# Optimization experiments

Measured on AMD Instinct MI355X. Metric: run time of the kernel, lower is better.

## Reference

```python
import jax, jax.numpy as jnp
import numpy as np

R = 15  # receptive-field rows (self.rfield)
_NAMES = ['1x', '2x', '3x', '4x', '1e', '2e', '3e', '4e', '5', '6', '7', '8', '9']
_CIN = [3, 64, 64, 64, 3, 64, 64, 64, 64, 64, 64, 64, 64]
_COUT = [64, 64, 64, 64, 64, 64, 64, 64, 64, 64, 64, 64, 3]


def _leaky(x):
    return jnp.where(x >= 0, x, 0.01 * x)  # nn.LeakyReLU default slope


def _conv(x, w, b, ph):
    # 3x3 conv, stride 1, padding (ph, 1) matching torch Conv2d padding=[ph, 1]
    y = jax.lax.conv_general_dilated(x, w, (1, 1), ((ph, ph), (1, 1)),
                                     dimension_numbers=('NCHW', 'OIHW', 'NCHW'))
    return y + b[None, :, None, None]


def setup_inputs():
    key = jax.random.key(0)
    ks = jax.random.split(key, len(_NAMES) + 1)
    inp = {'x': jax.random.normal(ks[0], (1, 3, 31, 256), jnp.float32)}
    for j, n in enumerate(_NAMES):
        std = np.float32((2.0 / (_CIN[j] * 9)) ** 0.5)  # He init for 3x3 conv
        inp['w' + n] = jax.random.normal(ks[j + 1], (_COUT[j], _CIN[j], 3, 3), jnp.float32) * std
        inp['b' + n] = jnp.zeros((_COUT[j],), jnp.float32)
    return inp


def _predict(s, e, p):
    # x-branch: 15 rows -> 9 rows (three H-valid convs)
    for n, ph in (('1x', 1), ('2x', 0), ('3x', 0), ('4x', 0)):
        s = _leaky(_conv(s, p['w' + n], p['b' + n], ph))
    # e-branch
    for n, ph in (('1e', 1), ('2e', 0), ('3e', 0), ('4e', 0)):
        e = _leaky(_conv(e, p['w' + n], p['b' + n], ph))
    B, C, Hs, W = s.shape  # C == 64 -> per-pixel 8x8 matrices; Hs == R - 6 == 9
    sr = jnp.transpose(s, (0, 2, 3, 1)).reshape(B, Hs, W, 8, 8)
    er = jnp.transpose(e, (0, 2, 3, 1)).reshape(B, Hs, W, 8, 8)
    pr = jnp.einsum('bhwij,bhwjk->bhwik', er, sr).reshape(B, Hs, W, 64)
    pr = jnp.transpose(pr, (0, 3, 1, 2))  # [B,64,9,W]
    # fuse stack: 9 rows -> 1 row, then 64 -> 3 channels
    for n, ph in (('5', 0), ('6', 0), ('7', 0), ('8', 0), ('9', 1)):
        pr = _leaky(_conv(pr, p['w' + n], p['b' + n], ph))
    return pr  # [B, 3, 1, W]


def _forward(x, p):
    B, C, H, W = x.shape

    def step(ebuf, i):
        # torch code sets error = x (alias), so slice_x and slice_e are the SAME mutated buffer
        sl = jax.lax.dynamic_slice(ebuf, (0, 0, i, 0), (B, C, R, W))
        pr = _predict(sl, sl, p)
        # act_row reads row ky of the (mutated) x, but row ky is overwritten only after this read,
        # so it still equals the original input row
        act = jax.lax.dynamic_slice(x, (0, 0, i + R, 0), (B, C, 1, W))
        ebuf = jax.lax.dynamic_update_slice(ebuf, act - pr, (0, 0, i + R, 0))
        return ebuf, pr

    ebuf, preds = jax.lax.scan(step, x, jnp.arange(H - R))
    pred = jnp.transpose(preds[:, :, :, 0, :], (1, 2, 0, 3))  # [S,B,C,1,W] -> [B,C,S,W]
    # 'truth' is read from the in-place-mutated x, i.e. the residual buffer, matching the torch aliasing bug/behavior
    truth = ebuf[:, :, R:, :]
    return pred, truth


def reference(x, w1x, b1x, w2x, b2x, w3x, b3x, w4x, b4x, w1e, b1e, w2e, b2e, w3e, b3e, w4e, b4e, w5, b5, w6, b6, w7, b7, w8, b8, w9, b9):
    p = dict(w1x=w1x, b1x=b1x, w2x=w2x, b2x=b2x, w3x=w3x, b3x=b3x, w4x=w4x, b4x=b4x,
             w1e=w1e, b1e=b1e, w2e=w2e, b2e=b2e, w3e=w3e, b3e=b3e, w4e=w4e, b4e=b4e,
             w5=w5, b5=b5, w6=w6, b6=b6, w7=w7, b7=b7, w8=w8, b8=b8, w9=w9, b9=b9)
    return _forward(x, p)
```

## Files before the change

### kernel.cpp

```cpp
#include <hip/hip_runtime.h>

#define LEAKY(v) ((v) >= 0.f ? (v) : 0.01f * (v))

#define CS   4608
#define ZS1  294912
#define TSL  16
#define BSL  17
#define EBCS 7936

struct JobD { const float* t0; const float* t1; const float* t2; float* o; };
struct IncP { JobD jd[6]; };

__global__ __launch_bounds__(256, 2) void convInc(
    IncP P, const float* __restrict__ W0, const float* __restrict__ B0,
    const float* __restrict__ W1, const float* __restrict__ B1,
    int zsel, int ics, int ocs)
{
    const int lane = threadIdx.x;
    const int y    = threadIdx.y;
    const int q    = blockIdx.x >> 6;
    const int cout = blockIdx.x & 63;
    const int z    = (zsel >> q) & 1;
    const float* W  = (z ? W1 : W0) + cout * 576 + y * 144;
    const float* Bv = z ? B1 : B0;
    const JobD jd  = P.jd[q];
    const int yo   = y * 16 * ics + lane * 4;
    const float* t0 = jd.t0 + yo;
    const float* t1 = jd.t1 + yo;
    const float* t2 = jd.t2 + yo;

    float acc[4] = {};
    #pragma unroll 4
    for (int c = 0; c < 16; ++c) {
        #pragma unroll
        for (int t = 0; t < 3; ++t) {
            const float* rp = (t == 0 ? t0 : (t == 1 ? t1 : t2)) + c * ics;
            float4 v = *(const float4*)rp;
            float wl = __shfl_up(v.w, 1);   if (lane == 0)  wl = 0.f;
            float wr = __shfl_down(v.x, 1); if (lane == 63) wr = 0.f;
            const float win[6] = {wl, v.x, v.y, v.z, v.w, wr};
            const float* wj = W + c * 9 + t * 3;
            #pragma unroll
            for (int cc = 0; cc < 4; ++cc)
                acc[cc] += wj[0] * win[cc] + wj[1] * win[cc + 1] + wj[2] * win[cc + 2];
        }
    }

    __shared__ float red[4][256];
    *(float4*)&red[y][lane * 4] = *(float4*)acc;
    __syncthreads();
    const int col = y * 64 + lane;
    float v = Bv[cout] + red[0][col] + red[1][col] + red[2][col] + red[3][col];
    jd.o[cout * ocs + col] = LEAKY(v);
}

struct C3P { const float* t[3][3]; float* o[3][2]; };

__global__ __launch_bounds__(256, 2) void conv3inc(
    C3P P, const float* __restrict__ W0, const float* __restrict__ B0,
    const float* __restrict__ W1, const float* __restrict__ B1)
{
    const int lane = threadIdx.x & 63;
    const int wv   = threadIdx.x >> 6;
    const int job  = blockIdx.x >> 3;
    const int cq   = blockIdx.x & 3;
    const int z    = (blockIdx.x >> 2) & 1;
    const int cout0 = __builtin_amdgcn_readfirstlane(cq * 16 + wv * 4);
    const float* W  = (z ? W1 : W0) + cout0 * 27;
    const float* Bv = z ? B1 : B0;

    float a[4][4] = {};
    #pragma unroll
    for (int t = 0; t < 3; ++t) {
        const float* rp = P.t[job][t];
        if (rp) {
            #pragma unroll
            for (int c = 0; c < 3; ++c) {
                float4 v = *(const float4*)(rp + c * EBCS + lane * 4);
                float wl = __shfl_up(v.w, 1);   if (lane == 0)  wl = 0.f;
                float wr = __shfl_down(v.x, 1); if (lane == 63) wr = 0.f;
                const float win[6] = {wl, v.x, v.y, v.z, v.w, wr};
                #pragma unroll
                for (int j = 0; j < 4; ++j) {
                    const float* wj = W + j * 27 + c * 9 + t * 3;
                    #pragma unroll
                    for (int cc = 0; cc < 4; ++cc)
                        a[j][cc] += wj[0] * win[cc] + wj[1] * win[cc + 1] + wj[2] * win[cc + 2];
                }
            }
        }
    }
    float* o = P.o[job][z];
    #pragma unroll
    for (int j = 0; j < 4; ++j) {
        const float bb = Bv[cout0 + j];
        float4 r4;
        r4.x = LEAKY(a[j][0] + bb); r4.y = LEAKY(a[j][1] + bb);
        r4.z = LEAKY(a[j][2] + bb); r4.w = LEAKY(a[j][3] + bb);
        *(float4*)(o + (cout0 + j) * CS + lane * 4) = r4;
    }
}

__global__ __launch_bounds__(256, 2) void conv3B(
    const float* __restrict__ ebuf,
    const float* __restrict__ W0, const float* __restrict__ B0,
    const float* __restrict__ W1, const float* __restrict__ B1,
    float* __restrict__ out)
{
    const int lane = threadIdx.x & 63;
    const int wv   = threadIdx.x >> 6;
    const int h  = blockIdx.y;
    const int cq = blockIdx.z & 3;
    const int z  = blockIdx.z >> 2;
    const int cout0 = __builtin_amdgcn_readfirstlane(cq * 16 + wv * 4);
    const float* W  = (z ? W1 : W0) + cout0 * 27;
    const float* Bv = z ? B1 : B0;

    float a[4][4] = {};
    #pragma unroll
    for (int kh = 0; kh < 3; ++kh) {
        const int r = h - 1 + kh;
        const bool valid = (r >= 0 && r < 15);
        const float msk = valid ? 1.f : 0.f;
        #pragma unroll
        for (int c = 0; c < 3; ++c) {
            const float* rr = ebuf + c * EBCS + (valid ? r : 0) * 256 + lane * 4;
            float4 v = *(const float4*)rr;
            v.x *= msk; v.y *= msk; v.z *= msk; v.w *= msk;
            float wl = __shfl_up(v.w, 1);   if (lane == 0)  wl = 0.f;
            float wr = __shfl_down(v.x, 1); if (lane == 63) wr = 0.f;
            const float win[6] = {wl, v.x, v.y, v.z, v.w, wr};
            #pragma unroll
            for (int j = 0; j < 4; ++j) {
                const float* wj = W + j * 27 + c * 9 + kh * 3;
                #pragma unroll
                for (int cc = 0; cc < 4; ++cc)
                    a[j][cc] += wj[0] * win[cc] + wj[1] * win[cc + 1] + wj[2] * win[cc + 2];
            }
        }
    }
    const int slot = (h == 0) ? TSL : (h == 14 ? BSL : (h & 15));
    float* o = out + (size_t)z * ZS1 + slot * 256;
    #pragma unroll
    for (int j = 0; j < 4; ++j) {
        const float bb = Bv[cout0 + j];
        float4 r4;
        r4.x = LEAKY(a[j][0] + bb); r4.y = LEAKY(a[j][1] + bb);
        r4.z = LEAKY(a[j][2] + bb); r4.w = LEAKY(a[j][3] + bb);
        *(float4*)(o + (cout0 + j) * CS + lane * 4) = r4;
    }
}

template<int HOUT, int HIN, int OFFI, int OFFO, int NZ>
__global__ __launch_bounds__(256, 2) void convYB(
    const float* __restrict__ in,
    const float* __restrict__ W0, const float* __restrict__ B0,
    const float* __restrict__ W1, const float* __restrict__ B1,
    float* __restrict__ out)
{
    const int lane = threadIdx.x;
    const int y    = threadIdx.y;
    const int h  = blockIdx.y;
    const int gz = blockIdx.z;
    const int z    = (NZ == 2) ? (gz >> 6) : 0;
    const int cout = (NZ == 2) ? (gz & 63) : gz;
    const float* W  = (z ? W1 : W0) + cout * 576 + y * 144;
    const float* Bv = z ? B1 : B0;
    const float* ib = in + (size_t)z * ZS1 + y * 16 * CS + lane * 4;

    int slot[3];
    #pragma unroll
    for (int t = 0; t < 3; ++t) {
        const int g = h + t;
        slot[t] = (g == 0) ? TSL : (g == HIN - 1 ? BSL : ((g + OFFI) & 15));
    }

    float acc[4] = {};
    #pragma unroll 4
    for (int c = 0; c < 16; ++c) {
        #pragma unroll
        for (int t = 0; t < 3; ++t) {
            float4 v = *(const float4*)(ib + c * CS + slot[t] * 256);
            float wl = __shfl_up(v.w, 1);   if (lane == 0)  wl = 0.f;
            float wr = __shfl_down(v.x, 1); if (lane == 63) wr = 0.f;
            const float win[6] = {wl, v.x, v.y, v.z, v.w, wr};
            const float* wj = W + c * 9 + t * 3;
            #pragma unroll
            for (int cc = 0; cc < 4; ++cc)
                acc[cc] += wj[0] * win[cc] + wj[1] * win[cc + 1] + wj[2] * win[cc + 2];
        }
    }

    __shared__ float red[4][256];
    *(float4*)&red[y][lane * 4] = *(float4*)acc;
    __syncthreads();
    const int col = y * 64 + lane;
    const int os = (h == 0) ? TSL : (h == HOUT - 1 ? BSL : ((h + OFFO) & 15));
    float v = Bv[cout] + red[0][col] + red[1][col] + red[2][col] + red[3][col];
    out[(size_t)z * ZS1 + cout * CS + os * 256 + col] = LEAKY(v);
}

__global__ __launch_bounds__(256, 2) void mmB(const float* __restrict__ L4R,
                                              float* __restrict__ MMR)
{
    const int col = threadIdx.x;
    const int r   = blockIdx.x;
    const int ig  = blockIdx.y;
    const int slot = (r == 0) ? TSL : (r == 8 ? BSL : ((r + 3) & 15));
    const float* s = L4R + slot * 256 + col;
    const float* e = L4R + ZS1 + slot * 256 + col;
    float sv[64];
    #pragma unroll
    for (int c = 0; c < 64; ++c) sv[c] = s[c * CS];
    float ev[8];
    #pragma unroll
    for (int j = 0; j < 8; ++j) ev[j] = e[(ig * 8 + j) * CS];
    #pragma unroll
    for (int k = 0; k < 8; ++k) {
        float acc = 0.f;
        #pragma unroll
        for (int j = 0; j < 8; ++j) acc += ev[j] * sv[j * 8 + k];
        MMR[(ig * 8 + k) * CS + slot * 256 + col] = acc;
    }
}

struct MMP { const float* s[3]; const float* e[3]; float* o[3]; };
__global__ __launch_bounds__(256, 2) void mminc(MMP P)
{
    const int col = threadIdx.x;
    const int job = blockIdx.x;
    const int ig  = blockIdx.y;
    const float* s = P.s[job] + col;
    const float* e = P.e[job] + col;
    float sv[64];
    #pragma unroll
    for (int c = 0; c < 64; ++c) sv[c] = s[c * CS];
    float ev[8];
    #pragma unroll
    for (int j = 0; j < 8; ++j) ev[j] = e[(ig * 8 + j) * CS];
    float* o = P.o[job];
    #pragma unroll
    for (int k = 0; k < 8; ++k) {
        float acc = 0.f;
        #pragma unroll
        for (int j = 0; j < 8; ++j) acc += ev[j] * sv[j * 8 + k];
        o[(ig * 8 + k) * CS + col] = acc;
    }
}

__global__ void conv9up(const float* __restrict__ pin, const float* __restrict__ w9,
                        const float* __restrict__ b9, const float* __restrict__ x,
                        float* __restrict__ ebuf, float* __restrict__ preds, int i)
{
    const int wcol = threadIdx.x;
    const int yq   = threadIdx.y;
    const int c0   = yq * 16;
    const bool mL = (wcol > 0), mR = (wcol < 255);
    float a0 = 0.f, a1 = 0.f, a2 = 0.f;

    #pragma unroll 4
    for (int c = 0; c < 16; ++c) {
        const int cin = c0 + c;
        const float* r_ = pin + cin * 256;
        float vm = mL ? r_[wcol - 1] : 0.f;
        float v0 = r_[wcol];
        float vp = mR ? r_[wcol + 1] : 0.f;
        const float* wk0 = w9 + (0 * 64 + cin) * 9 + 3;
        const float* wk1 = w9 + (1 * 64 + cin) * 9 + 3;
        const float* wk2 = w9 + (2 * 64 + cin) * 9 + 3;
        a0 += vm * wk0[0] + v0 * wk0[1] + vp * wk0[2];
        a1 += vm * wk1[0] + v0 * wk1[1] + vp * wk1[2];
        a2 += vm * wk2[0] + v0 * wk2[1] + vp * wk2[2];
    }

    __shared__ float red[4][3][256];
    red[yq][0][wcol] = a0;
    red[yq][1][wcol] = a1;
    red[yq][2][wcol] = a2;
    __syncthreads();

    if (yq == 0) {
        #pragma unroll
        for (int j = 0; j < 3; ++j) {
            float v = b9[j] + red[0][j][wcol] + red[1][j][wcol]
                            + red[2][j][wcol] + red[3][j][wcol];
            v = LEAKY(v);
            preds[i * 768 + j * 256 + wcol] = v;
            ebuf[j * EBCS + (15 + i) * 256 + wcol] =
                x[j * EBCS + (15 + i) * 256 + wcol] - v;
        }
    }
}

__global__ void finalize(const float* __restrict__ preds, const float* __restrict__ ebuf,
                         float* __restrict__ o)
{
    const int idx = blockIdx.x * 256 + threadIdx.x;
    if (idx >= 24576) return;
    if (idx < 12288) {
        const int c = idx >> 12;
        const int t = (idx >> 8) & 15;
        const int w = idx & 255;
        o[idx] = preds[t * 768 + c * 256 + w];
    } else {
        const int j = idx - 12288;
        const int c = j >> 12;
        const int t = (j >> 8) & 15;
        const int w = j & 255;
        o[idx] = ebuf[c * EBCS + (15 + t) * 256 + w];
    }
}

extern "C" void kernel_launch(void* const* d_in, const int* in_sizes, int n_in,
                              void* d_out, int out_size, void* d_ws, size_t ws_size,
                              hipStream_t stream)
{
    const float* x   = (const float*)d_in[0];
    const float* w1x = (const float*)d_in[1];  const float* b1x = (const float*)d_in[2];
    const float* w2x = (const float*)d_in[3];  const float* b2x = (const float*)d_in[4];
    const float* w3x = (const float*)d_in[5];  const float* b3x = (const float*)d_in[6];
    const float* w4x = (const float*)d_in[7];  const float* b4x = (const float*)d_in[8];
    const float* w1e = (const float*)d_in[9];  const float* b1e = (const float*)d_in[10];
    const float* w2e = (const float*)d_in[11]; const float* b2e = (const float*)d_in[12];
    const float* w3e = (const float*)d_in[13]; const float* b3e = (const float*)d_in[14];
    const float* w4e = (const float*)d_in[15]; const float* b4e = (const float*)d_in[16];
    const float* w5  = (const float*)d_in[17]; const float* b5  = (const float*)d_in[18];
    const float* w6  = (const float*)d_in[19]; const float* b6  = (const float*)d_in[20];
    const float* w7  = (const float*)d_in[21]; const float* b7  = (const float*)d_in[22];
    const float* w8  = (const float*)d_in[23]; const float* b8  = (const float*)d_in[24];
    const float* w9  = (const float*)d_in[25]; const float* b9  = (const float*)d_in[26];

    float* ws    = (float*)d_ws;
    float* ebuf  = ws;
    float* L1R   = ebuf + 23808;
    float* L2R   = L1R + 589824;
    float* L3R   = L2R + 589824;
    float* L4R   = L3R + 589824;
    float* MMR   = L4R + 589824;
    float* L5R   = MMR + 294912;
    float* L6R   = L5R + 294912;
    float* L7b   = L6R + 294912;
    float* L8b   = L7b + 49152;
    float* preds = L8b + 16384;

    auto S2 = [](int c) { return c & 15; };
    auto r2 = [](float* b, int z, int slot) { return b + (size_t)z * ZS1 + slot * 256; };
    auto r1 = [](float* b, int slot) { return b + slot * 256; };

    hipMemcpyAsync(ebuf, x, 23808 * sizeof(float), hipMemcpyDeviceToDevice, stream);

    const dim3 cb(64, 4);

    conv3B<<<dim3(1, 15, 8), 256, 0, stream>>>(ebuf, w1x, b1x, w1e, b1e, L1R);
    convYB<13, 15, 0, 1, 2><<<dim3(1, 13, 128), cb, 0, stream>>>(L1R, w2x, b2x, w2e, b2e, L2R);
    convYB<11, 13, 1, 2, 2><<<dim3(1, 11, 128), cb, 0, stream>>>(L2R, w3x, b3x, w3e, b3e, L3R);
    convYB<9, 11, 2, 3, 2><<<dim3(1, 9, 128), cb, 0, stream>>>(L3R, w4x, b4x, w4e, b4e, L4R);
    mmB<<<dim3(9, 8), 256, 0, stream>>>(L4R, MMR);
    convYB<7, 9, 3, 4, 1><<<dim3(1, 7, 64), cb, 0, stream>>>(MMR, w5, b5, w5, b5, L5R);
    convYB<5, 7, 4, 5, 1><<<dim3(1, 5, 64), cb, 0, stream>>>(L5R, w6, b6, w6, b6, L6R);

    for (int i = 0; i < 16; ++i) {
        if (i > 0) {
            C3P p3 = {};
            p3.t[0][0] = nullptr;                p3.t[0][1] = ebuf + i * 256;        p3.t[0][2] = ebuf + (i + 1) * 256;
            p3.t[1][0] = ebuf + (i + 13) * 256;  p3.t[1][1] = ebuf + (i + 14) * 256; p3.t[1][2] = nullptr;
            p3.t[2][0] = ebuf + (i + 12) * 256;  p3.t[2][1] = ebuf + (i + 13) * 256; p3.t[2][2] = ebuf + (i + 14) * 256;
            for (int z = 0; z < 2; ++z) {
                p3.o[0][z] = r2(L1R, z, TSL);
                p3.o[1][z] = r2(L1R, z, BSL);
                p3.o[2][z] = r2(L1R, z, S2(i + 13));
            }
            conv3inc<<<24, 256, 0, stream>>>(p3, w1x, b1x, w1e, b1e);

            IncP p2 = {};
            for (int z = 0; z < 2; ++z) {
                p2.jd[0 * 2 + z] = { r2(L1R, z, TSL),        r2(L1R, z, S2(i + 1)),  r2(L1R, z, S2(i + 2)),  r2(L2R, z, TSL) };
                p2.jd[1 * 2 + z] = { r2(L1R, z, S2(i + 12)), r2(L1R, z, S2(i + 13)), r2(L1R, z, BSL),        r2(L2R, z, BSL) };
                p2.jd[2 * 2 + z] = { r2(L1R, z, S2(i + 11)), r2(L1R, z, S2(i + 12)), r2(L1R, z, S2(i + 13)), r2(L2R, z, S2(i + 12)) };
            }
            convInc<<<384, cb, 0, stream>>>(p2, w2x, b2x, w2e, b2e, 42, CS, CS);

            IncP p3i = {};
            for (int z = 0; z < 2; ++z) {
                p3i.jd[0 * 2 + z] = { r2(L2R, z, TSL),        r2(L2R, z, S2(i + 2)),  r2(L2R, z, S2(i + 3)),  r2(L3R, z, TSL) };
                p3i.jd[1 * 2 + z] = { r2(L2R, z, S2(i + 11)), r2(L2R, z, S2(i + 12)), r2(L2R, z, BSL),        r2(L3R, z, BSL) };
                p3i.jd[2 * 2 + z] = { r2(L2R, z, S2(i + 10)), r2(L2R, z, S2(i + 11)), r2(L2R, z, S2(i + 12)), r2(L3R, z, S2(i + 11)) };
            }
            convInc<<<384, cb, 0, stream>>>(p3i, w3x, b3x, w3e, b3e, 42, CS, CS);

            IncP p4 = {};
            for (int z = 0; z < 2; ++z) {
                p4.jd[0 * 2 + z] = { r2(L3R, z, TSL),        r2(L3R, z, S2(i + 3)),  r2(L3R, z, S2(i + 4)),  r2(L4R, z, TSL) };
                p4.jd[1 * 2 + z] = { r2(L3R, z, S2(i + 10)), r2(L3R, z, S2(i + 11)), r2(L3R, z, BSL),        r2(L4R, z, BSL) };
                p4.jd[2 * 2 + z] = { r2(L3R, z, S2(i + 9)),  r2(L3R, z, S2(i + 10)), r2(L3R, z, S2(i + 11)), r2(L4R, z, S2(i + 10)) };
            }
            convInc<<<384, cb, 0, stream>>>(p4, w4x, b4x, w4e, b4e, 42, CS, CS);

            MMP pm;
            pm.s[0] = r2(L4R, 0, TSL);        pm.e[0] = r2(L4R, 1, TSL);        pm.o[0] = r1(MMR, TSL);
            pm.s[1] = r2(L4R, 0, BSL);        pm.e[1] = r2(L4R, 1, BSL);        pm.o[1] = r1(MMR, BSL);
            pm.s[2] = r2(L4R, 0, S2(i + 10)); pm.e[2] = r2(L4R, 1, S2(i + 10)); pm.o[2] = r1(MMR, S2(i + 10));
            mminc<<<dim3(3, 8), 256, 0, stream>>>(pm);

            IncP p5 = {};
            p5.jd[0] = { r1(MMR, TSL),       r1(MMR, S2(i + 4)),  r1(MMR, S2(i + 5)),  r1(L5R, TSL) };
            p5.jd[1] = { r1(MMR, S2(i + 9)), r1(MMR, S2(i + 10)), r1(MMR, BSL),        r1(L5R, BSL) };
            p5.jd[2] = { r1(MMR, S2(i + 8)), r1(MMR, S2(i + 9)),  r1(MMR, S2(i + 10)), r1(L5R, S2(i + 9)) };
            convInc<<<192, cb, 0, stream>>>(p5, w5, b5, w5, b5, 0, CS, CS);

            IncP p6 = {};
            p6.jd[0] = { r1(L5R, TSL),       r1(L5R, S2(i + 5)), r1(L5R, S2(i + 6)), r1(L6R, TSL) };
            p6.jd[1] = { r1(L5R, S2(i + 8)), r1(L5R, S2(i + 9)), r1(L5R, BSL),       r1(L6R, BSL) };
            p6.jd[2] = { r1(L5R, S2(i + 7)), r1(L5R, S2(i + 8)), r1(L5R, S2(i + 9)), r1(L6R, S2(i + 8)) };
            convInc<<<192, cb, 0, stream>>>(p6, w6, b6, w6, b6, 0, CS, CS);
        }

        IncP p7 = {};
        p7.jd[0] = { r1(L6R, TSL),       r1(L6R, S2(i + 6)), r1(L6R, S2(i + 7)), L7b };
        p7.jd[1] = { r1(L6R, S2(i + 6)), r1(L6R, S2(i + 7)), r1(L6R, S2(i + 8)), L7b + 256 };
        p7.jd[2] = { r1(L6R, S2(i + 7)), r1(L6R, S2(i + 8)), r1(L6R, BSL),       L7b + 512 };
        convInc<<<192, cb, 0, stream>>>(p7, w7, b7, w7, b7, 0, CS, 768);

        IncP p8 = {};
        p8.jd[0] = { L7b, L7b + 256, L7b + 512, L8b };
        convInc<<<64, cb, 0, stream>>>(p8, w8, b8, w8, b8, 0, 768, 256);

        conv9up<<<dim3(1, 1, 1), dim3(256, 4), 0, stream>>>(L8b, w9, b9, x, ebuf, preds, i);
    }

    finalize<<<96, 256, 0, stream>>>(preds, ebuf, (float*)d_out);
}
```

Baseline: 1.905 ms.

## Fuse conv9 into layer-1 kernel and per-pixel matmul into layer-5 conv

Each step's conv9/residual update is now recomputed redundantly in every block of a new fused layer-1 kernel, which feeds the new residual row through shared memory. The per-pixel 8x8 matmul is folded into the layer-5 conv kernel, so each block recomputes the product rows it needs into a large shared buffer. Block 0 and one designated block write the results back to global memory. This removes two launches per step and their serialization, at the cost of redundant compute, a 64 KB+ shared allocation that limits occupancy, and more scattered global reads in fusedL5.

```diff
diff --git a/kernel.cpp b/kernel.cpp
--- a/kernel.cpp
+++ b/kernel.cpp
@@ -7,6 +7,7 @@
 #define TSL  16
 #define BSL  17
 #define EBCS 7936
+#define S16(c) ((c) & 15)
 
 struct JobD { const float* t0; const float* t1; const float* t2; float* o; };
 struct IncP { JobD jd[6]; };
@@ -54,29 +55,79 @@
     jd.o[cout * ocs + col] = LEAKY(v);
 }
 
-struct C3P { const float* t[3][3]; float* o[3][2]; };
-
-__global__ __launch_bounds__(256, 2) void conv3inc(
-    C3P P, const float* __restrict__ W0, const float* __restrict__ B0,
-    const float* __restrict__ W1, const float* __restrict__ B1)
-{
-    const int lane = threadIdx.x & 63;
-    const int wv   = threadIdx.x >> 6;
+__global__ __launch_bounds__(256, 2) void fusedL1(
+    const float* __restrict__ L8b, const float* __restrict__ w9,
+    const float* __restrict__ b9, const float* __restrict__ x,
+    float* __restrict__ ebuf, float* __restrict__ preds,
+    const float* __restrict__ W0, const float* __restrict__ B0,
+    const float* __restrict__ W1, const float* __restrict__ B1,
+    float* __restrict__ L1R, int i)
+{
+    __shared__ float eL[3][256];
+    const int tx = threadIdx.x;
+
+    {
+        const int col = tx;
+        const bool mL = (col > 0), mR = (col < 255);
+        float a0 = 0.f, a1 = 0.f, a2 = 0.f;
+        #pragma unroll 4
+        for (int cin = 0; cin < 64; ++cin) {
+            const float* r_ = L8b + cin * 256;
+            float vm = mL ? r_[col - 1] : 0.f;
+            float v0 = r_[col];
+            float vp = mR ? r_[col + 1] : 0.f;
+            const float* wk0 = w9 + (0 * 64 + cin) * 9 + 3;
+            const float* wk1 = w9 + (1 * 64 + cin) * 9 + 3;
+            const float* wk2 = w9 + (2 * 64 + cin) * 9 + 3;
+            a0 += vm * wk0[0] + v0 * wk0[1] + vp * wk0[2];
+            a1 += vm * wk1[0] + v0 * wk1[1] + vp * wk1[2];
+            a2 += vm * wk2[0] + v0 * wk2[1] + vp * wk2[2];
+        }
+        const float pv[3] = {LEAKY(b9[0] + a0), LEAKY(b9[1] + a1), LEAKY(b9[2] + a2)};
+        #pragma unroll
+        for (int j = 0; j < 3; ++j) {
+            const float e = x[j * EBCS + (i + 14) * 256 + col] - pv[j];
+            eL[j][col] = e;
+            if (blockIdx.x == 0) {
+                preds[(i - 1) * 768 + j * 256 + col] = pv[j];
+                ebuf[j * EBCS + (i + 14) * 256 + col] = e;
+            }
+        }
+    }
+    __syncthreads();
+
+    const int lane = tx & 63;
+    const int wv   = tx >> 6;
     const int job  = blockIdx.x >> 3;
     const int cq   = blockIdx.x & 3;
     const int z    = (blockIdx.x >> 2) & 1;
-    const int cout0 = __builtin_amdgcn_readfirstlane(cq * 16 + wv * 4);
+    const int cout0 = cq * 16 + wv * 4;
     const float* W  = (z ? W1 : W0) + cout0 * 27;
     const float* Bv = z ? B1 : B0;
 
+    const float* tp[3] = {nullptr, nullptr, nullptr};
+    int st[3] = {EBCS, EBCS, EBCS};
+    int os;
+    if (job == 0) {
+        tp[1] = ebuf + i * 256;        tp[2] = ebuf + (i + 1) * 256;
+        os = TSL;
+    } else if (job == 1) {
+        tp[0] = ebuf + (i + 13) * 256; tp[1] = &eL[0][0]; st[1] = 256;
+        os = BSL;
+    } else {
+        tp[0] = ebuf + (i + 12) * 256; tp[1] = ebuf + (i + 13) * 256;
+        tp[2] = &eL[0][0]; st[2] = 256;
+        os = S16(i + 13);
+    }
+
     float a[4][4] = {};
     #pragma unroll
     for (int t = 0; t < 3; ++t) {
-        const float* rp = P.t[job][t];
+        const float* rp = tp[t];
         if (rp) {
             #pragma unroll
             for (int c = 0; c < 3; ++c) {
-                float4 v = *(const float4*)(rp + c * EBCS + lane * 4);
+                float4 v = *(const float4*)(rp + c * st[t] + lane * 4);
                 float wl = __shfl_up(v.w, 1);   if (lane == 0)  wl = 0.f;
                 float wr = __shfl_down(v.x, 1); if (lane == 63) wr = 0.f;
                 const float win[6] = {wl, v.x, v.y, v.z, v.w, wr};
@@ -90,7 +141,7 @@
             }
         }
     }
-    float* o = P.o[job][z];
+    float* o = L1R + (size_t)z * ZS1 + os * 256;
     #pragma unroll
     for (int j = 0; j < 4; ++j) {
         const float bb = Bv[cout0 + j];
@@ -101,6 +152,97 @@
     }
 }
 
+__global__ __launch_bounds__(256, 2) void fusedL5(
+    const float* __restrict__ L4R, float* __restrict__ MMR,
+    const float* __restrict__ W, const float* __restrict__ B,
+    float* __restrict__ L5R, int i)
+{
+    __shared__ float rowbuf[64 * 256];
+    __shared__ float red[4][256];
+    const int lane = threadIdx.x, y = threadIdx.y;
+    const int cout = blockIdx.x & 63, jt = blockIdx.x >> 6;
+    const float* Wc = W + cout * 576 + y * 144;
+
+    int kind[3], slot[3], os;
+    if (jt == 0) {
+        kind[0] = 1; slot[0] = TSL;
+        kind[1] = 0; slot[1] = S16(i + 4);
+        kind[2] = 0; slot[2] = S16(i + 5);
+        os = TSL;
+    } else if (jt == 1) {
+        kind[0] = 0; slot[0] = S16(i + 9);
+        kind[1] = 1; slot[1] = S16(i + 10);
+        kind[2] = 1; slot[2] = BSL;
+        os = BSL;
+    } else {
+        kind[0] = 0; slot[0] = S16(i + 8);
+        kind[1] = 0; slot[1] = S16(i + 9);
+        kind[2] = 1; slot[2] = S16(i + 10);
+        os = S16(i + 9);
+    }
+
+    float acc[4] = {};
+    #pragma unroll
+    for (int t = 0; t < 3; ++t) {
+        const float* base;
+        int str;
+        if (kind[t] == 0) {
+            base = MMR + slot[t] * 256;
+            str = CS;
+        } else {
+            const float* sB = L4R + slot[t] * 256;
+            const float* eB = L4R + ZS1 + slot[t] * 256;
+            #pragma unroll
+            for (int h = 0; h < 2; ++h) {
+                const int i8 = y * 2 + h;
+                float4 e4[8];
+                #pragma unroll
+                for (int j = 0; j < 8; ++j)
+                    e4[j] = *(const float4*)(eB + (i8 * 8 + j) * CS + lane * 4);
+                #pragma unroll
+                for (int k = 0; k < 8; ++k) {
+                    float4 o4 = {0.f, 0.f, 0.f, 0.f};
+                    #pragma unroll
+                    for (int j = 0; j < 8; ++j) {
+                        float4 s4 = *(const float4*)(sB + (j * 8 + k) * CS + lane * 4);
+                        o4.x += e4[j].x * s4.x; o4.y += e4[j].y * s4.y;
+                        o4.z += e4[j].z * s4.z; o4.w += e4[j].w * s4.w;
+                    }
+                    *(float4*)&rowbuf[(i8 * 8 + k) * 256 + lane * 4] = o4;
+                }
+            }
+            if (jt == 2 && cout == 0) {
+                #pragma unroll
+                for (int c = 0; c < 16; ++c) {
+                    const int ch = y * 16 + c;
+                    *(float4*)(MMR + ch * CS + S16(i + 10) * 256 + lane * 4) =
+                        *(const float4*)&rowbuf[ch * 256 + lane * 4];
+                }
+            }
+            base = rowbuf;
+            str = 256;
+        }
+        #pragma unroll 4
+        for (int c = 0; c < 16; ++c) {
+            const float* rp = base + (y * 16 + c) * str + lane * 4;
+            float4 v = *(const float4*)rp;
+            float wl = __shfl_up(v.w, 1);   if (lane == 0)  wl = 0.f;
+            float wr = __shfl_down(v.x, 1); if (lane == 63) wr = 0.f;
+            const float win[6] = {wl, v.x, v.y, v.z, v.w, wr};
+            const float* wj = Wc + c * 9 + t * 3;
+            #pragma unroll
+            for (int cc = 0; cc < 4; ++cc)
+                acc[cc] += wj[0] * win[cc] + wj[1] * win[cc + 1] + wj[2] * win[cc + 2];
+        }
+    }
+
+    *(float4*)&red[y][lane * 4] = *(float4*)acc;
+    __syncthreads();
+    const int col = y * 64 + lane;
+    float v = B[cout] + red[0][col] + red[1][col] + red[2][col] + red[3][col];
+    L5R[cout * CS + os * 256 + col] = LEAKY(v);
+}
+
 __global__ __launch_bounds__(256, 2) void conv3B(
     const float* __restrict__ ebuf,
     const float* __restrict__ W0, const float* __restrict__ B0,
@@ -112,7 +254,7 @@
     const int h  = blockIdx.y;
     const int cq = blockIdx.z & 3;
     const int z  = blockIdx.z >> 2;
-    const int cout0 = __builtin_amdgcn_readfirstlane(cq * 16 + wv * 4);
+    const int cout0 = cq * 16 + wv * 4;
     const float* W  = (z ? W1 : W0) + cout0 * 27;
     const float* Bv = z ? B1 : B0;
 
@@ -224,30 +366,6 @@
     }
 }
 
-struct MMP { const float* s[3]; const float* e[3]; float* o[3]; };
-__global__ __launch_bounds__(256, 2) void mminc(MMP P)
-{
-    const int col = threadIdx.x;
-    const int job = blockIdx.x;
-    const int ig  = blockIdx.y;
-    const float* s = P.s[job] + col;
-    const float* e = P.e[job] + col;
-    float sv[64];
-    #pragma unroll
-    for (int c = 0; c < 64; ++c) sv[c] = s[c * CS];
-    float ev[8];
-    #pragma unroll
-    for (int j = 0; j < 8; ++j) ev[j] = e[(ig * 8 + j) * CS];
-    float* o = P.o[job];
-    #pragma unroll
-    for (int k = 0; k < 8; ++k) {
-        float acc = 0.f;
-        #pragma unroll
-        for (int j = 0; j < 8; ++j) acc += ev[j] * sv[j * 8 + k];
-        o[(ig * 8 + k) * CS + col] = acc;
-    }
-}
-
 __global__ void conv9up(const float* __restrict__ pin, const float* __restrict__ w9,
                         const float* __restrict__ b9, const float* __restrict__ x,
                         float* __restrict__ ebuf, float* __restrict__ preds, int i)
@@ -359,74 +477,65 @@
     convYB<7, 9, 3, 4, 1><<<dim3(1, 7, 64), cb, 0, stream>>>(MMR, w5, b5, w5, b5, L5R);
     convYB<5, 7, 4, 5, 1><<<dim3(1, 5, 64), cb, 0, stream>>>(L5R, w6, b6, w6, b6, L6R);
 
-    for (int i = 0; i < 16; ++i) {
-        if (i > 0) {
-            C3P p3 = {};
-            p3.t[0][0] = nullptr;                p3.t[0][1] = ebuf + i * 256;        p3.t[0][2] = ebuf + (i + 1) * 256;
-            p3.t[1][0] = ebuf + (i + 13) * 256;  p3.t[1][1] = ebuf + (i + 14) * 256; p3.t[1][2] = nullptr;
-            p3.t[2][0] = ebuf + (i + 12) * 256;  p3.t[2][1] = ebuf + (i + 13) * 256; p3.t[2][2] = ebuf + (i + 14) * 256;
-            for (int z = 0; z < 2; ++z) {
-                p3.o[0][z] = r2(L1R, z, TSL);
-                p3.o[1][z] = r2(L1R, z, BSL);
-                p3.o[2][z] = r2(L1R, z, S2(i + 13));
-            }
-            conv3inc<<<24, 256, 0, stream>>>(p3, w1x, b1x, w1e, b1e);
-
-            IncP p2 = {};
-            for (int z = 0; z < 2; ++z) {
-                p2.jd[0 * 2 + z] = { r2(L1R, z, TSL),        r2(L1R, z, S2(i + 1)),  r2(L1R, z, S2(i + 2)),  r2(L2R, z, TSL) };
-                p2.jd[1 * 2 + z] = { r2(L1R, z, S2(i + 12)), r2(L1R, z, S2(i + 13)), r2(L1R, z, BSL),        r2(L2R, z, BSL) };
-                p2.jd[2 * 2 + z] = { r2(L1R, z, S2(i + 11)), r2(L1R, z, S2(i + 12)), r2(L1R, z, S2(i + 13)), r2(L2R, z, S2(i + 12)) };
-            }
-            convInc<<<384, cb, 0, stream>>>(p2, w2x, b2x, w2e, b2e, 42, CS, CS);
-
-            IncP p3i = {};
-            for (int z = 0; z < 2; ++z) {
-                p3i.jd[0 * 2 + z] = { r2(L2R, z, TSL),        r2(L2R, z, S2(i + 2)),  r2(L2R, z, S2(i + 3)),  r2(L3R, z, TSL) };
-                p3i.jd[1 * 2 + z] = { r2(L2R, z, S2(i + 11)), r2(L2R, z, S2(i + 12)), r2(L2R, z, BSL),        r2(L3R, z, BSL) };
-                p3i.jd[2 * 2 + z] = { r2(L2R, z, S2(i + 10)), r2(L2R, z, S2(i + 11)), r2(L2R, z, S2(i + 12)), r2(L3R, z, S2(i + 11)) };
-            }
-            convInc<<<384, cb, 0, stream>>>(p3i, w3x, b3x, w3e, b3e, 42, CS, CS);
-
-            IncP p4 = {};
-            for (int z = 0; z < 2; ++z) {
-                p4.jd[0 * 2 + z] = { r2(L3R, z, TSL),        r2(L3R, z, S2(i + 3)),  r2(L3R, z, S2(i + 4)),  r2(L4R, z, TSL) };
-                p4.jd[1 * 2 + z] = { r2(L3R, z, S2(i + 10)), r2(L3R, z, S2(i + 11)), r2(L3R, z, BSL),        r2(L4R, z, BSL) };
-                p4.jd[2 * 2 + z] = { r2(L3R, z, S2(i + 9)),  r2(L3R, z, S2(i + 10)), r2(L3R, z, S2(i + 11)), r2(L4R, z, S2(i + 10)) };
-            }
-            convInc<<<384, cb, 0, stream>>>(p4, w4x, b4x, w4e, b4e, 42, CS, CS);
-
-            MMP pm;
-            pm.s[0] = r2(L4R, 0, TSL);        pm.e[0] = r2(L4R, 1, TSL);        pm.o[0] = r1(MMR, TSL);
-            pm.s[1] = r2(L4R, 0, BSL);        pm.e[1] = r2(L4R, 1, BSL);        pm.o[1] = r1(MMR, BSL);
-            pm.s[2] = r2(L4R, 0, S2(i + 10)); pm.e[2] = r2(L4R, 1, S2(i + 10)); pm.o[2] = r1(MMR, S2(i + 10));
-            mminc<<<dim3(3, 8), 256, 0, stream>>>(pm);
-
-            IncP p5 = {};
-            p5.jd[0] = { r1(MMR, TSL),       r1(MMR, S2(i + 4)),  r1(MMR, S2(i + 5)),  r1(L5R, TSL) };
-            p5.jd[1] = { r1(MMR, S2(i + 9)), r1(MMR, S2(i + 10)), r1(MMR, BSL),        r1(L5R, BSL) };
-            p5.jd[2] = { r1(MMR, S2(i + 8)), r1(MMR, S2(i + 9)),  r1(MMR, S2(i + 10)), r1(L5R, S2(i + 9)) };
-            convInc<<<192, cb, 0, stream>>>(p5, w5, b5, w5, b5, 0, CS, CS);
-
-            IncP p6 = {};
-            p6.jd[0] = { r1(L5R, TSL),       r1(L5R, S2(i + 5)), r1(L5R, S2(i + 6)), r1(L6R, TSL) };
-            p6.jd[1] = { r1(L5R, S2(i + 8)), r1(L5R, S2(i + 9)), r1(L5R, BSL),       r1(L6R, BSL) };
-            p6.jd[2] = { r1(L5R, S2(i + 7)), r1(L5R, S2(i + 8)), r1(L5R, S2(i + 9)), r1(L6R, S2(i + 8)) };
-            convInc<<<192, cb, 0, stream>>>(p6, w6, b6, w6, b6, 0, CS, CS);
-        }
-
+    {
+        const int i = 0;
         IncP p7 = {};
         p7.jd[0] = { r1(L6R, TSL),       r1(L6R, S2(i + 6)), r1(L6R, S2(i + 7)), L7b };
         p7.jd[1] = { r1(L6R, S2(i + 6)), r1(L6R, S2(i + 7)), r1(L6R, S2(i + 8)), L7b + 256 };
         p7.jd[2] = { r1(L6R, S2(i + 7)), r1(L6R, S2(i + 8)), r1(L6R, BSL),       L7b + 512 };
         convInc<<<192, cb, 0, stream>>>(p7, w7, b7, w7, b7, 0, CS, 768);
-
         IncP p8 = {};
         p8.jd[0] = { L7b, L7b + 256, L7b + 512, L8b };
         convInc<<<64, cb, 0, stream>>>(p8, w8, b8, w8, b8, 0, 768, 256);
-
-        conv9up<<<dim3(1, 1, 1), dim3(256, 4), 0, stream>>>(L8b, w9, b9, x, ebuf, preds, i);
-    }
-
+    }
+
+    for (int i = 1; i < 16; ++i) {
+        fusedL1<<<24, 256, 0, stream>>>(L8b, w9, b9, x, ebuf, preds,
+                                        w1x, b1x, w1e, b1e, L1R, i);
+
+        IncP p2 = {};
+        for (int z = 0; z < 2; ++z) {
+            p2.jd[0 * 2 + z] = { r2(L1R, z, TSL),        r2(L1R, z, S2(i + 1)),  r2(L1R, z, S2(i + 2)),  r2(L2R, z, TSL) };
+            p2.jd[1 * 2 + z] = { r2(L1R, z, S2(i + 12)), r2(L1R, z, S2(i + 13)), r2(L1R, z, BSL),        r2(L2R, z, BSL) };
+            p2.jd[2 * 2 + z] = { r2(L1R, z, S2(i + 11)), r2(L1R, z, S2(i + 12)), r2(L1R, z, S2(i + 13)), r2(L2R, z, S2(i + 12)) };
+        }
+        convInc<<<384, cb, 0, stream>>>(p2, w2x, b2x, w2e, b2e, 42, CS, CS);
+
+        IncP p3i = {};
+        for (int z = 0; z < 2; ++z) {
+            p3i.jd[0 * 2 + z] = { r2(L2R, z, TSL),        r2(L2R, z, S2(i + 2)),  r2(L2R, z, S2(i + 3)),  r2(L3R, z, TSL) };
+            p3i.jd[1 * 2 + z] = { r2(L2R, z, S2(i + 11)), r2(L2R, z, S2(i + 12)), r2(L2R, z, BSL),        r2(L3R, z, BSL) };
+            p3i.jd[2 * 2 + z] = { r2(L2R, z, S2(i + 10)), r2(L2R, z, S2(i + 11)), r2(L2R, z, S2(i + 12)), r2(L3R, z, S2(i + 11)) };
+        }
+        convInc<<<384, cb, 0, stream>>>(p3i, w3x, b3x, w3e, b3e, 42, CS, CS);
+
+        IncP p4 = {};
+        for (int z = 0; z < 2; ++z) {
+            p4.jd[0 * 2 + z] = { r2(L3R, z, TSL),        r2(L3R, z, S2(i + 3)),  r2(L3R, z, S2(i + 4)),  r2(L4R, z, TSL) };
+            p4.jd[1 * 2 + z] = { r2(L3R, z, S2(i + 10)), r2(L3R, z, S2(i + 11)), r2(L3R, z, BSL),        r2(L4R, z, BSL) };
+            p4.jd[2 * 2 + z] = { r2(L3R, z, S2(i + 9)),  r2(L3R, z, S2(i + 10)), r2(L3R, z, S2(i + 11)), r2(L4R, z, S2(i + 10)) };
+        }
+        convInc<<<384, cb, 0, stream>>>(p4, w4x, b4x, w4e, b4e, 42, CS, CS);
+
+        fusedL5<<<192, cb, 0, stream>>>(L4R, MMR, w5, b5, L5R, i);
+
+        IncP p6 = {};
+        p6.jd[0] = { r1(L5R, TSL),       r1(L5R, S2(i + 5)), r1(L5R, S2(i + 6)), r1(L6R, TSL) };
+        p6.jd[1] = { r1(L5R, S2(i + 8)), r1(L5R, S2(i + 9)), r1(L5R, BSL),       r1(L6R, BSL) };
+        p6.jd[2] = { r1(L5R, S2(i + 7)), r1(L5R, S2(i + 8)), r1(L5R, S2(i + 9)), r1(L6R, S2(i + 8)) };
+        convInc<<<192, cb, 0, stream>>>(p6, w6, b6, w6, b6, 0, CS, CS);
+
+        IncP p7 = {};
+        p7.jd[0] = { r1(L6R, TSL),       r1(L6R, S2(i + 6)), r1(L6R, S2(i + 7)), L7b };
+        p7.jd[1] = { r1(L6R, S2(i + 6)), r1(L6R, S2(i + 7)), r1(L6R, S2(i + 8)), L7b + 256 };
+        p7.jd[2] = { r1(L6R, S2(i + 7)), r1(L6R, S2(i + 8)), r1(L6R, BSL),       L7b + 512 };
+        convInc<<<192, cb, 0, stream>>>(p7, w7, b7, w7, b7, 0, CS, 768);
+
+        IncP p8 = {};
+        p8.jd[0] = { L7b, L7b + 256, L7b + 512, L8b };
+        convInc<<<64, cb, 0, stream>>>(p8, w8, b8, w8, b8, 0, 768, 256);
+    }
+
+    conv9up<<<dim3(1, 1, 1), dim3(256, 4), 0, stream>>>(L8b, w9, b9, x, ebuf, preds, 15);
     finalize<<<96, 256, 0, stream>>>(preds, ebuf, (float*)d_out);
 }
```

Result: slower. 2.725 ms (+43.0%).
